# Kernel tuning notes

Measured on AMD Instinct MI355X. Metric: run time of the kernel, lower is better.

Reference implementation:

```python
import jax, jax.numpy as jnp
import numpy as np

S = 16384   # num src nodes
D = 16384   # num dst nodes
FS = 128    # src feature len
FD = 128    # dst feature len
R = 50.0    # dist threshold (m)
L = 2005.0  # box side so avg degree ~ 32
LN_EPS = 1e-5


def setup_inputs() -> dict:
    rng = np.random.default_rng(0)
    src_pos_np = rng.uniform(0.0, L, (S, 2)).astype(np.float32)
    dst_pos_np = rng.uniform(0.0, L, (D, 2)).astype(np.float32)
    # radius-graph edge construction (data-dependent, done once outside jit)
    es, ed = [], []
    CH = 2048
    for i in range(0, S, CH):
        d = np.linalg.norm(src_pos_np[i:i + CH, None, :] - dst_pos_np[None, :, :], axis=-1)
        si, di = np.nonzero(d <= R)
        es.append((si + i).astype(np.int32))
        ed.append(di.astype(np.int32))
    edge_src_idx = jnp.asarray(np.concatenate(es))
    edge_dst_idx = jnp.asarray(np.concatenate(ed))

    key = jax.random.key(0)
    ks = jax.random.split(key, 12)
    w = lambda k, shape: (jax.random.normal(k, shape, jnp.float32) * 0.02)
    return {
        'src_node_features': jax.random.normal(ks[0], (S, FS), jnp.float32),
        'src_node_pos': jnp.asarray(src_pos_np),
        'dst_node_features': jax.random.normal(ks[1], (D, FD), jnp.float32),
        'dst_node_pos': jnp.asarray(dst_pos_np),
        'src_w': w(ks[2], (FS, FS)), 'src_b': jnp.zeros((FS,), jnp.float32),
        'dst_w': w(ks[3], (FD, FD)), 'dst_b': jnp.zeros((FD,), jnp.float32),
        'dist_w': w(ks[4], (2, FD)), 'dist_b': jnp.zeros((FD,), jnp.float32),
        'edge_w1': w(ks[5], (FS + FD + FD, FD)), 'edge_b1': jnp.zeros((FD,), jnp.float32),
        'edge_w2': w(ks[6], (FD, FD)), 'edge_b2': jnp.zeros((FD,), jnp.float32),
        'ln_g': jnp.ones((FD,), jnp.float32), 'ln_b': jnp.zeros((FD,), jnp.float32),
        'out_w': w(ks[7], (FD, FD)), 'out_b': jnp.zeros((FD,), jnp.float32),
        'edge_src_idx': edge_src_idx,
        'edge_dst_idx': edge_dst_idx,
    }


def reference(src_node_features, src_node_pos, dst_node_features, dst_node_pos,
              src_w, src_b, dst_w, dst_b, dist_w, dist_b,
              edge_w1, edge_b1, edge_w2, edge_b2, ln_g, ln_b, out_w, out_b,
              edge_src_idx, edge_dst_idx):
    # node encoders: Linear + ReLU
    src_enc = jax.nn.relu(src_node_features @ src_w + src_b)   # [S, FS]
    dst_enc = jax.nn.relu(dst_node_features @ dst_w + dst_b)   # [D, FD]
    # gather per-edge
    e_src = src_enc[edge_src_idx]                               # [E, FS]
    e_dst = dst_enc[edge_dst_idx]                               # [E, FD]
    e_dpos = src_node_pos[edge_src_idx] - dst_node_pos[edge_dst_idx]  # [E, 2]
    e_dist = jax.nn.relu(e_dpos @ dist_w + dist_b)              # [E, FD]
    # edge MLP: Linear-ReLU-Linear on concat [E, FS+FD+FD]
    e_in = jnp.concatenate([e_src, e_dist, e_dst], axis=-1)
    e_out = jax.nn.relu(e_in @ edge_w1 + edge_b1) @ edge_w2 + edge_b2  # [E, FD]
    # scatter-add to destination nodes
    agg = dst_enc + jax.ops.segment_sum(e_out, edge_dst_idx, num_segments=D)
    # LayerNorm + ReLU + Linear + residual + ReLU
    mu = jnp.mean(agg, axis=-1, keepdims=True)
    var = jnp.mean(jnp.square(agg - mu), axis=-1, keepdims=True)
    ln = (agg - mu) * jax.lax.rsqrt(var + LN_EPS) * ln_g + ln_b
    h = jax.nn.relu(ln) @ out_w + out_b + dst_node_features
    return jax.nn.relu(h)
```

## Files before the change

### kernel.cpp

```cpp
#include <hip/hip_runtime.h>

typedef unsigned short ushort_t;
typedef unsigned int uint_t;
typedef short bhalf8 __attribute__((ext_vector_type(8)));
typedef float f32x4 __attribute__((ext_vector_type(4)));

__device__ __forceinline__ float b2f(ushort_t u) {
    union { uint_t i; float f; } v; v.i = ((uint_t)u) << 16; return v.f;
}
__device__ __forceinline__ ushort_t f2b(float f) {
    union { float f; uint_t i; } v; v.f = f;
    uint_t r = v.i + 0x7fffu + ((v.i >> 16) & 1u);
    return (ushort_t)(r >> 16);
}
__device__ __forceinline__ uint_t addpack_trunc(uint_t a, uint_t b) {
    union { uint_t i; float f; } t0, t1, s0, s1;
    t0.i = a << 16;          s0.i = b << 16;
    t1.i = a & 0xffff0000u;  s1.i = b & 0xffff0000u;
    float lo = t0.f + s0.f, hi = t1.f + s1.f;
    union { float f; uint_t i; } rl, rh; rl.f = lo; rh.f = hi;
    return (rl.i >> 16) | (rh.i & 0xffff0000u);
}

__global__ __launch_bounds__(256) void prep_kernel(
    const float* __restrict__ wsrc, const float* __restrict__ wdst,
    const float* __restrict__ w2,   const float* __restrict__ wout,
    const float* __restrict__ w1,
    ushort_t* __restrict__ msrc, ushort_t* __restrict__ mdst,
    ushort_t* __restrict__ m2,   ushort_t* __restrict__ mout,
    ushort_t* __restrict__ m1a,  ushort_t* __restrict__ m1b,
    ushort_t* __restrict__ m1c,
    const int* __restrict__ edi, int E, int* __restrict__ deg,
    float* __restrict__ hsum, int countB, int zeroB, int Dn)
{
    int b = blockIdx.x, tid = threadIdx.x;
    if (b < 56) {
        const float* ins[7] = { wsrc, wdst, w2, wout, w1, w1 + 128*128, w1 + 256*128 };
        ushort_t* outs[7]   = { msrc, mdst, m2, mout, m1a, m1b, m1c };
        int mat = b >> 3;
        const float* in = ins[mat];
        ushort_t* out = outs[mat];
        int flat = (b & 7)*256 + tid;
        int nt = flat >> 8, rem = flat & 255;
        int ks = rem >> 6, lane = rem & 63;
        int q = lane >> 4, m = lane & 15;
        #pragma unroll
        for (int j = 0; j < 8; ++j)
            out[flat*8 + j] = f2b(in[(ks*32 + q*8 + j)*128 + nt*16 + m]);
    } else if (b < 56 + countB) {
        int i = (b - 56)*256 + tid;
        if (i < E) atomicAdd(&deg[edi[i]], 1);
    } else {
        int zb = b - 56 - countB;
        float4* h4 = (float4*)hsum;
        int total4 = Dn*32;
        for (int i = zb*256 + tid; i < total4; i += zeroB*256)
            h4[i] = make_float4(0.f, 0.f, 0.f, 0.f);
    }
}

__global__ __launch_bounds__(256) void enc2_kernel(
    const float* __restrict__ src_feat, const float* __restrict__ dst_feat,
    const ushort_t* __restrict__ msrc, const ushort_t* __restrict__ mdst,
    const ushort_t* __restrict__ m1a,  const ushort_t* __restrict__ m1c,
    const float* __restrict__ src_b,   const float* __restrict__ dst_b,
    ushort_t* __restrict__ Csrc, ushort_t* __restrict__ Cdst,
    ushort_t* __restrict__ dst_enc, int Sb)
{
    __shared__ ushort_t A_l[64*136];
    __shared__ ushort_t E_l[64*136];
    __shared__ float b_l[128];
    int tid = threadIdx.x, blk = blockIdx.x;

    const float* A; const ushort_t *W1m, *W2m; const float* bias;
    ushort_t *outC, *outEnc; int rowbase;
    if (blk < Sb) { A = src_feat; W1m = msrc; W2m = m1a; bias = src_b;
                    outC = Csrc; outEnc = nullptr; rowbase = blk*64; }
    else          { A = dst_feat; W1m = mdst; W2m = m1c; bias = dst_b;
                    outC = Cdst; outEnc = dst_enc; rowbase = (blk - Sb)*64; }

    const float4* A4 = (const float4*)A;
    for (int i = tid; i < 2048; i += 256) {
        int r = i >> 5, c = i & 31;
        float4 v = A4[(size_t)(rowbase + r)*32 + c];
        uint2 u;
        u.x = (uint_t)f2b(v.x) | ((uint_t)f2b(v.y) << 16);
        u.y = (uint_t)f2b(v.z) | ((uint_t)f2b(v.w) << 16);
        *(uint2*)(A_l + r*136 + c*4) = u;
    }
    if (tid < 128) b_l[tid] = bias[tid];
    __syncthreads();

    int lane = tid & 63, w = tid >> 6, q = lane >> 4, m = lane & 15;
    const bhalf8* Wv1 = (const bhalf8*)W1m;
    f32x4 acc[4][2] = {};
    #pragma unroll
    for (int ks = 0; ks < 4; ++ks) {
        bhalf8 bf0 = Wv1[((2*w)*4 + ks)*64 + lane];
        bhalf8 bf1 = Wv1[((2*w+1)*4 + ks)*64 + lane];
        #pragma unroll
        for (int mt = 0; mt < 4; ++mt) {
            bhalf8 a = *(const bhalf8*)(A_l + (mt*16 + m)*136 + ks*32 + q*8);
            acc[mt][0] = __builtin_amdgcn_mfma_f32_16x16x32_bf16(a, bf0, acc[mt][0], 0, 0, 0);
            acc[mt][1] = __builtin_amdgcn_mfma_f32_16x16x32_bf16(a, bf1, acc[mt][1], 0, 0, 0);
        }
    }
    #pragma unroll
    for (int mt = 0; mt < 4; ++mt)
    #pragma unroll
    for (int nt = 0; nt < 2; ++nt)
    #pragma unroll
    for (int reg = 0; reg < 4; ++reg) {
        int col = w*32 + nt*16 + m;
        int row = mt*16 + q*4 + reg;
        ushort_t e = f2b(fmaxf(acc[mt][nt][reg] + b_l[col], 0.f));
        E_l[row*136 + col] = e;
        if (outEnc) outEnc[(size_t)(rowbase + row)*128 + col] = e;
    }
    __syncthreads();

    const bhalf8* Wv2 = (const bhalf8*)W2m;
    f32x4 acc2[4][2] = {};
    #pragma unroll
    for (int ks = 0; ks < 4; ++ks) {
        bhalf8 bf0 = Wv2[((2*w)*4 + ks)*64 + lane];
        bhalf8 bf1 = Wv2[((2*w+1)*4 + ks)*64 + lane];
        #pragma unroll
        for (int mt = 0; mt < 4; ++mt) {
            bhalf8 a = *(const bhalf8*)(E_l + (mt*16 + m)*136 + ks*32 + q*8);
            acc2[mt][0] = __builtin_amdgcn_mfma_f32_16x16x32_bf16(a, bf0, acc2[mt][0], 0, 0, 0);
            acc2[mt][1] = __builtin_amdgcn_mfma_f32_16x16x32_bf16(a, bf1, acc2[mt][1], 0, 0, 0);
        }
    }
    #pragma unroll
    for (int mt = 0; mt < 4; ++mt)
    #pragma unroll
    for (int nt = 0; nt < 2; ++nt)
    #pragma unroll
    for (int reg = 0; reg < 4; ++reg) {
        int col = w*32 + nt*16 + m;
        int row = mt*16 + q*4 + reg;
        outC[(size_t)(rowbase + row)*128 + col] = f2b(acc2[mt][nt][reg]);
    }
}

__global__ __launch_bounds__(1024) void scan_deg(const int* __restrict__ deg,
                                                 int* __restrict__ nxt, int Dn)
{
    __shared__ int sums[1024];
    int t = threadIdx.x;
    int per = Dn >> 10;
    const int4* d4 = (const int4*)(deg + t*per);
    int4 v[4]; int s = 0;
    #pragma unroll
    for (int k = 0; k < 4; ++k) { v[k] = d4[k]; s += v[k].x + v[k].y + v[k].z + v[k].w; }
    sums[t] = s;
    __syncthreads();
    for (int off = 1; off < 1024; off <<= 1) {
        int x = (t >= off) ? sums[t - off] : 0;
        __syncthreads();
        sums[t] += x;
        __syncthreads();
    }
    int run = sums[t] - s;
    int4* n4 = (int4*)(nxt + t*per);
    #pragma unroll
    for (int k = 0; k < 4; ++k) {
        int4 o;
        o.x = run; run += v[k].x;
        o.y = run; run += v[k].y;
        o.z = run; run += v[k].z;
        o.w = run; run += v[k].w;
        n4[k] = o;
    }
}

__global__ __launch_bounds__(256) void fill_sorted(
    const int* __restrict__ esi, const int* __restrict__ edi, int E,
    int* __restrict__ nxt, int* __restrict__ ss, int* __restrict__ sd)
{
    int i = blockIdx.x*256 + threadIdx.x;
    if (i < E) {
        int s = esi[i], d = edi[i];
        int p = atomicAdd(&nxt[d], 1);
        ss[p] = s; sd[p] = d;
    }
}

__global__ __launch_bounds__(256, 4) void edge_kernel(
    const ushort_t* __restrict__ Csrc, const ushort_t* __restrict__ Cdst,
    const float* __restrict__ src_pos, const float* __restrict__ dst_pos,
    const int* __restrict__ sorted_s, const int* __restrict__ sorted_d, int E,
    const ushort_t* __restrict__ w1bm, const float* __restrict__ eb1,
    const float* __restrict__ dist_w, const float* __restrict__ dist_b,
    float* __restrict__ hsum)
{
    __shared__ ushort_t X[64*136];
    __shared__ ushort_t G_l[64*136];
    __shared__ int s_l[64], ed_l[64], dv_l[64];
    __shared__ float dx_l[64], dy_l[64];
    __shared__ float b1_l[128], dw0_l[128], dw1_l[128], db_l[128];

    int tid = threadIdx.x, blk = blockIdx.x;

    if (tid < 64) {
        int slot = blk*64 + tid;
        if (slot < E) {
            int s = sorted_s[slot], d = sorted_d[slot];
            s_l[tid] = s; ed_l[tid] = d; dv_l[tid] = d;
            float2 sp = ((const float2*)src_pos)[s];
            float2 dp = ((const float2*)dst_pos)[d];
            dx_l[tid] = sp.x - dp.x;
            dy_l[tid] = sp.y - dp.y;
        } else {
            s_l[tid] = 0; ed_l[tid] = 0x7fffffff; dv_l[tid] = 0;
            dx_l[tid] = 0.f; dy_l[tid] = 0.f;
        }
    }
    if (tid < 128) {
        b1_l[tid]  = eb1[tid];
        dw0_l[tid] = dist_w[tid];
        dw1_l[tid] = dist_w[128 + tid];
        db_l[tid]  = dist_b[tid];
    }
    __syncthreads();

    const uint4* cs4 = (const uint4*)Csrc;
    const uint4* cd4 = (const uint4*)Cdst;
    for (int i = tid; i < 1024; i += 256) {
        int r = i >> 4, c = i & 15;
        uint4 a = cs4[(size_t)s_l[r]*16 + c];
        uint4 b = cd4[(size_t)dv_l[r]*16 + c];
        uint4 u;
        u.x = addpack_trunc(a.x, b.x);
        u.y = addpack_trunc(a.y, b.y);
        u.z = addpack_trunc(a.z, b.z);
        u.w = addpack_trunc(a.w, b.w);
        *(uint4*)(G_l + r*136 + c*8) = u;
    }
    for (int i = tid; i < 4096; i += 256) {
        int r = i >> 6, j2 = (i & 63)*2;
        float dx = dx_l[r], dy = dy_l[r];
        float v0 = fmaxf(dx*dw0_l[j2]   + dy*dw1_l[j2]   + db_l[j2],   0.f);
        float v1 = fmaxf(dx*dw0_l[j2+1] + dy*dw1_l[j2+1] + db_l[j2+1], 0.f);
        *(uint_t*)(X + r*136 + j2) = (uint_t)f2b(v0) | ((uint_t)f2b(v1) << 16);
    }
    __syncthreads();

    int lane = tid & 63, w = tid >> 6, q = lane >> 4, m = lane & 15;
    f32x4 acc[4][2] = {};
    const bhalf8* Wv = (const bhalf8*)w1bm;
    #pragma unroll
    for (int ks = 0; ks < 4; ++ks) {
        bhalf8 bf0 = Wv[((2*w)*4 + ks)*64 + lane];
        bhalf8 bf1 = Wv[((2*w+1)*4 + ks)*64 + lane];
        #pragma unroll
        for (int mt = 0; mt < 4; ++mt) {
            bhalf8 a = *(const bhalf8*)(X + (mt*16 + m)*136 + ks*32 + q*8);
            acc[mt][0] = __builtin_amdgcn_mfma_f32_16x16x32_bf16(a, bf0, acc[mt][0], 0, 0, 0);
            acc[mt][1] = __builtin_amdgcn_mfma_f32_16x16x32_bf16(a, bf1, acc[mt][1], 0, 0, 0);
        }
    }
    __syncthreads();

    #pragma unroll
    for (int mt = 0; mt < 4; ++mt)
    #pragma unroll
    for (int reg = 0; reg < 4; ++reg) {
        int row = mt*16 + q*4 + reg;
        #pragma unroll
        for (int nt = 0; nt < 2; ++nt) {
            int col = w*32 + nt*16 + m;
            float v = acc[mt][nt][reg] + b1_l[col] + b2f(G_l[row*136 + col]);
            X[row*136 + col] = f2b(fmaxf(v, 0.f));
        }
    }
    __syncthreads();

    {
        int j = tid & 127, h = tid >> 7;
        int rend = h*32 + 32;
        float a = 0.f;
        for (int r = h*32; r < rend; ++r) {
            a += b2f(X[r*136 + j]);
            int dcur = ed_l[r];
            bool bnd = (r == rend - 1) || (ed_l[r + 1] != dcur);
            if (bnd) {
                if (dcur != 0x7fffffff) atomicAdd(&hsum[(size_t)dcur*128 + j], a);
                a = 0.f;
            }
        }
    }
}

__global__ __launch_bounds__(256) void aggfinal_kernel(
    const float* __restrict__ hsum, const ushort_t* __restrict__ w2m,
    const float* __restrict__ b2, const int* __restrict__ deg,
    const ushort_t* __restrict__ dst_enc, const float* __restrict__ ln_g,
    const float* __restrict__ ln_b, const ushort_t* __restrict__ moutm,
    const float* __restrict__ out_b, const float* __restrict__ dst_feat,
    float* __restrict__ out)
{
    __shared__ char buf[64*132*4];
    __shared__ ushort_t act_l[64*136];
    __shared__ float b2_l[128], g_l[128], bl_l[128], ob_l[128];
    __shared__ int deg_l[64];
    __shared__ float ps[64][4], ps2[64][4], mu_l[64], inv_l[64];

    ushort_t* A_l = (ushort_t*)buf;
    float* Y = (float*)buf;
    int tid = threadIdx.x, blk = blockIdx.x;

    const float4* hv = (const float4*)hsum;
    for (int i = tid; i < 1024; i += 256) {
        int r = i >> 4, c = i & 15;
        size_t base = (size_t)(blk*64 + r)*32 + c*2;
        float4 p0 = hv[base], p1 = hv[base + 1];
        uint4 u;
        u.x = (uint_t)f2b(p0.x) | ((uint_t)f2b(p0.y) << 16);
        u.y = (uint_t)f2b(p0.z) | ((uint_t)f2b(p0.w) << 16);
        u.z = (uint_t)f2b(p1.x) | ((uint_t)f2b(p1.y) << 16);
        u.w = (uint_t)f2b(p1.z) | ((uint_t)f2b(p1.w) << 16);
        *(uint4*)(A_l + r*136 + c*8) = u;
    }
    if (tid < 128) { b2_l[tid] = b2[tid]; g_l[tid] = ln_g[tid];
                     bl_l[tid] = ln_b[tid]; ob_l[tid] = out_b[tid]; }
    if (tid < 64) deg_l[tid] = deg[blk*64 + tid];
    __syncthreads();

    int lane = tid & 63, w = tid >> 6, q = lane >> 4, m = lane & 15;
    f32x4 acc[4][2] = {};
    const bhalf8* Wv = (const bhalf8*)w2m;
    #pragma unroll
    for (int ks = 0; ks < 4; ++ks) {
        bhalf8 bf0 = Wv[((2*w)*4 + ks)*64 + lane];
        bhalf8 bf1 = Wv[((2*w+1)*4 + ks)*64 + lane];
        #pragma unroll
        for (int mt = 0; mt < 4; ++mt) {
            bhalf8 a = *(const bhalf8*)(A_l + (mt*16 + m)*136 + ks*32 + q*8);
            acc[mt][0] = __builtin_amdgcn_mfma_f32_16x16x32_bf16(a, bf0, acc[mt][0], 0, 0, 0);
            acc[mt][1] = __builtin_amdgcn_mfma_f32_16x16x32_bf16(a, bf1, acc[mt][1], 0, 0, 0);
        }
    }
    __syncthreads();

    #pragma unroll
    for (int mt = 0; mt < 4; ++mt)
    #pragma unroll
    for (int nt = 0; nt < 2; ++nt)
    #pragma unroll
    for (int reg = 0; reg < 4; ++reg) {
        int col = w*32 + nt*16 + m;
        int rowl = mt*16 + q*4 + reg;
        size_t grow = (size_t)blk*64 + rowl;
        float v = acc[mt][nt][reg] + (float)deg_l[rowl]*b2_l[col] + b2f(dst_enc[grow*128 + col]);
        Y[rowl*132 + col] = v;
    }
    __syncthreads();

    {
        int r = tid >> 2, t4 = tid & 3;
        float s = 0.f, s2 = 0.f;
        for (int jj = 0; jj < 32; ++jj) {
            float v = Y[r*132 + t4*32 + jj];
            s += v; s2 += v*v;
        }
        ps[r][t4] = s; ps2[r][t4] = s2;
    }
    __syncthreads();
    if (tid < 64) {
        int r = tid;
        float sum = ps[r][0] + ps[r][1] + ps[r][2] + ps[r][3];
        float sum2 = ps2[r][0] + ps2[r][1] + ps2[r][2] + ps2[r][3];
        float mu = sum / 128.f;
        float var = sum2 / 128.f - mu*mu;
        mu_l[r] = mu;
        inv_l[r] = 1.0f / sqrtf(var + 1e-5f);
    }
    __syncthreads();
    for (int i = tid; i < 4096; i += 256) {
        int r = i >> 6, j2 = (i & 63)*2;
        float v0 = fmaxf((Y[r*132 + j2]   - mu_l[r]) * inv_l[r] * g_l[j2]   + bl_l[j2],   0.f);
        float v1 = fmaxf((Y[r*132 + j2+1] - mu_l[r]) * inv_l[r] * g_l[j2+1] + bl_l[j2+1], 0.f);
        *(uint_t*)(act_l + r*136 + j2) = (uint_t)f2b(v0) | ((uint_t)f2b(v1) << 16);
    }
    __syncthreads();

    f32x4 acc2[4][2] = {};
    const bhalf8* Wo = (const bhalf8*)moutm;
    #pragma unroll
    for (int ks = 0; ks < 4; ++ks) {
        bhalf8 bf0 = Wo[((2*w)*4 + ks)*64 + lane];
        bhalf8 bf1 = Wo[((2*w+1)*4 + ks)*64 + lane];
        #pragma unroll
        for (int mt = 0; mt < 4; ++mt) {
            bhalf8 a = *(const bhalf8*)(act_l + (mt*16 + m)*136 + ks*32 + q*8);
            acc2[mt][0] = __builtin_amdgcn_mfma_f32_16x16x32_bf16(a, bf0, acc2[mt][0], 0, 0, 0);
            acc2[mt][1] = __builtin_amdgcn_mfma_f32_16x16x32_bf16(a, bf1, acc2[mt][1], 0, 0, 0);
        }
    }
    #pragma unroll
    for (int mt = 0; mt < 4; ++mt)
    #pragma unroll
    for (int nt = 0; nt < 2; ++nt)
    #pragma unroll
    for (int reg = 0; reg < 4; ++reg) {
        int col = w*32 + nt*16 + m;
        size_t row = (size_t)blk*64 + mt*16 + q*4 + reg;
        float v = acc2[mt][nt][reg] + ob_l[col] + dst_feat[row*128 + col];
        out[row*128 + col] = fmaxf(v, 0.f);
    }
}

extern "C" void kernel_launch(void* const* d_in, const int* in_sizes, int n_in,
                              void* d_out, int out_size, void* d_ws, size_t ws_size,
                              hipStream_t stream)
{
    const float* src_feat = (const float*)d_in[0];
    const float* src_pos  = (const float*)d_in[1];
    const float* dst_feat = (const float*)d_in[2];
    const float* dst_pos  = (const float*)d_in[3];
    const float* src_w    = (const float*)d_in[4];
    const float* src_b    = (const float*)d_in[5];
    const float* dst_w    = (const float*)d_in[6];
    const float* dst_b    = (const float*)d_in[7];
    const float* dist_w   = (const float*)d_in[8];
    const float* dist_b   = (const float*)d_in[9];
    const float* w1       = (const float*)d_in[10];
    const float* b1       = (const float*)d_in[11];
    const float* w2       = (const float*)d_in[12];
    const float* b2       = (const float*)d_in[13];
    const float* ln_g     = (const float*)d_in[14];
    const float* ln_b     = (const float*)d_in[15];
    const float* out_w    = (const float*)d_in[16];
    const float* out_b    = (const float*)d_in[17];
    const int* esi        = (const int*)d_in[18];
    const int* edi        = (const int*)d_in[19];
    int E = in_sizes[18];
    int S = in_sizes[0] / 128;
    int D = in_sizes[2] / 128;

    char* ws = (char*)d_ws;
    size_t off = 0;
    auto alloc = [&](size_t bytes) { char* p = ws + off; off += (bytes + 511) & ~(size_t)511; return p; };
    ushort_t* Csrc    = (ushort_t*)alloc((size_t)S*128*2);
    ushort_t* Cdst    = (ushort_t*)alloc((size_t)D*128*2);
    ushort_t* dst_enc = (ushort_t*)alloc((size_t)D*128*2);
    float*    hsum    = (float*)   alloc((size_t)D*128*4);
    ushort_t* msrc    = (ushort_t*)alloc(128*128*2);
    ushort_t* mdst    = (ushort_t*)alloc(128*128*2);
    ushort_t* m2      = (ushort_t*)alloc(128*128*2);
    ushort_t* mout    = (ushort_t*)alloc(128*128*2);
    ushort_t* m1a     = (ushort_t*)alloc(128*128*2);
    ushort_t* m1b     = (ushort_t*)alloc(128*128*2);
    ushort_t* m1c     = (ushort_t*)alloc(128*128*2);
    int*      deg     = (int*)     alloc((size_t)D*4);
    int*      nxt     = (int*)     alloc((size_t)D*4);
    int*      ss      = (int*)     alloc((size_t)E*4);
    int*      sd      = (int*)     alloc((size_t)E*4);

    hipMemsetAsync(deg, 0, (size_t)D*4, stream);

    int countB = (E + 255)/256;
    int zeroB = 256;
    prep_kernel<<<56 + countB + zeroB, 256, 0, stream>>>(
        src_w, dst_w, w2, out_w, w1,
        msrc, mdst, m2, mout, m1a, m1b, m1c,
        edi, E, deg, hsum, countB, zeroB, D);

    int Sb = S/64, Db = D/64;
    enc2_kernel<<<Sb + Db, 256, 0, stream>>>(
        src_feat, dst_feat, msrc, mdst, m1a, m1c, src_b, dst_b,
        Csrc, Cdst, dst_enc, Sb);

    scan_deg<<<1, 1024, 0, stream>>>(deg, nxt, D);
    fill_sorted<<<(E + 255)/256, 256, 0, stream>>>(esi, edi, E, nxt, ss, sd);

    edge_kernel<<<(E + 63)/64, 256, 0, stream>>>(
        Csrc, Cdst, src_pos, dst_pos, ss, sd, E,
        m1b, b1, dist_w, dist_b, hsum);

    aggfinal_kernel<<<Db, 256, 0, stream>>>(
        hsum, m2, b2, deg, dst_enc, ln_g, ln_b,
        mout, out_b, dst_feat, (float*)d_out);
}
```

Baseline: 247.5 us.

## Fuse degree scan into encoder, pack sorted edges, keep edge hidden in fp32 LDS

Folds the single-block degree prefix scan into the encoder launch as an extra block, removing one kernel launch. Moves the edge bias b1 into the precomputed dst-side projection, and stores the sorted (src,dst) pairs as one int2 array. In the edge kernel, the ReLU hidden values are kept in fp32 shared memory aliased over the X/G buffers instead of being rounded back to bf16, and segment boundaries and destination offsets are precomputed once per block. The scan block now uses 256 threads with 16 int4 loads each, and the distance features use truncating bf16 packing, which slightly changes rounding.

```diff
diff --git a/kernel.cpp b/kernel.cpp
--- a/kernel.cpp
+++ b/kernel.cpp
@@ -13,13 +13,17 @@
     uint_t r = v.i + 0x7fffu + ((v.i >> 16) & 1u);
     return (ushort_t)(r >> 16);
 }
+__device__ __forceinline__ uint_t f2u(float f) {
+    union { float f; uint_t i; } v; v.f = f; return v.i;
+}
+__device__ __forceinline__ uint_t pack_trunc(float lo, float hi) {
+    return (f2u(lo) >> 16) | (f2u(hi) & 0xffff0000u);
+}
 __device__ __forceinline__ uint_t addpack_trunc(uint_t a, uint_t b) {
     union { uint_t i; float f; } t0, t1, s0, s1;
     t0.i = a << 16;          s0.i = b << 16;
     t1.i = a & 0xffff0000u;  s1.i = b & 0xffff0000u;
-    float lo = t0.f + s0.f, hi = t1.f + s1.f;
-    union { float f; uint_t i; } rl, rh; rl.f = lo; rh.f = hi;
-    return (rl.i >> 16) | (rh.i & 0xffff0000u);
+    return pack_trunc(t0.f + s0.f, t1.f + s1.f);
 }
 
 __global__ __launch_bounds__(256) void prep_kernel(
@@ -64,20 +68,54 @@
     const ushort_t* __restrict__ msrc, const ushort_t* __restrict__ mdst,
     const ushort_t* __restrict__ m1a,  const ushort_t* __restrict__ m1c,
     const float* __restrict__ src_b,   const float* __restrict__ dst_b,
+    const float* __restrict__ b1,
     ushort_t* __restrict__ Csrc, ushort_t* __restrict__ Cdst,
-    ushort_t* __restrict__ dst_enc, int Sb)
+    ushort_t* __restrict__ dst_enc,
+    const int* __restrict__ deg, int* __restrict__ nxt, int Dn,
+    int Sb, int Db)
 {
+    int tid = threadIdx.x, blk = blockIdx.x;
+
+    if (blk == Sb + Db) {
+        __shared__ int sums[256];
+        int per = Dn >> 8;
+        const int4* d4 = (const int4*)(deg + tid*per);
+        int4 v[16]; int s = 0;
+        #pragma unroll
+        for (int k = 0; k < 16; ++k) { v[k] = d4[k]; s += v[k].x + v[k].y + v[k].z + v[k].w; }
+        sums[tid] = s;
+        __syncthreads();
+        for (int off = 1; off < 256; off <<= 1) {
+            int x = (tid >= off) ? sums[tid - off] : 0;
+            __syncthreads();
+            sums[tid] += x;
+            __syncthreads();
+        }
+        int run = sums[tid] - s;
+        int4* n4 = (int4*)(nxt + tid*per);
+        #pragma unroll
+        for (int k = 0; k < 16; ++k) {
+            int4 o;
+            o.x = run; run += v[k].x;
+            o.y = run; run += v[k].y;
+            o.z = run; run += v[k].z;
+            o.w = run; run += v[k].w;
+            n4[k] = o;
+        }
+        return;
+    }
+
     __shared__ ushort_t A_l[64*136];
     __shared__ ushort_t E_l[64*136];
     __shared__ float b_l[128];
-    int tid = threadIdx.x, blk = blockIdx.x;
+    __shared__ float b2_l[128];
 
     const float* A; const ushort_t *W1m, *W2m; const float* bias;
-    ushort_t *outC, *outEnc; int rowbase;
+    ushort_t *outC, *outEnc; int rowbase; const float* bias2;
     if (blk < Sb) { A = src_feat; W1m = msrc; W2m = m1a; bias = src_b;
-                    outC = Csrc; outEnc = nullptr; rowbase = blk*64; }
+                    outC = Csrc; outEnc = nullptr; rowbase = blk*64; bias2 = nullptr; }
     else          { A = dst_feat; W1m = mdst; W2m = m1c; bias = dst_b;
-                    outC = Cdst; outEnc = dst_enc; rowbase = (blk - Sb)*64; }
+                    outC = Cdst; outEnc = dst_enc; rowbase = (blk - Sb)*64; bias2 = b1; }
 
     const float4* A4 = (const float4*)A;
     for (int i = tid; i < 2048; i += 256) {
@@ -88,7 +126,7 @@
         u.y = (uint_t)f2b(v.z) | ((uint_t)f2b(v.w) << 16);
         *(uint2*)(A_l + r*136 + c*4) = u;
     }
-    if (tid < 128) b_l[tid] = bias[tid];
+    if (tid < 128) { b_l[tid] = bias[tid]; b2_l[tid] = bias2 ? bias2[tid] : 0.f; }
     __syncthreads();
 
     int lane = tid & 63, w = tid >> 6, q = lane >> 4, m = lane & 15;
@@ -140,91 +178,68 @@
     for (int reg = 0; reg < 4; ++reg) {
         int col = w*32 + nt*16 + m;
         int row = mt*16 + q*4 + reg;
-        outC[(size_t)(rowbase + row)*128 + col] = f2b(acc2[mt][nt][reg]);
-    }
-}
-
-__global__ __launch_bounds__(1024) void scan_deg(const int* __restrict__ deg,
-                                                 int* __restrict__ nxt, int Dn)
-{
-    __shared__ int sums[1024];
-    int t = threadIdx.x;
-    int per = Dn >> 10;
-    const int4* d4 = (const int4*)(deg + t*per);
-    int4 v[4]; int s = 0;
-    #pragma unroll
-    for (int k = 0; k < 4; ++k) { v[k] = d4[k]; s += v[k].x + v[k].y + v[k].z + v[k].w; }
-    sums[t] = s;
-    __syncthreads();
-    for (int off = 1; off < 1024; off <<= 1) {
-        int x = (t >= off) ? sums[t - off] : 0;
-        __syncthreads();
-        sums[t] += x;
-        __syncthreads();
-    }
-    int run = sums[t] - s;
-    int4* n4 = (int4*)(nxt + t*per);
-    #pragma unroll
-    for (int k = 0; k < 4; ++k) {
-        int4 o;
-        o.x = run; run += v[k].x;
-        o.y = run; run += v[k].y;
-        o.z = run; run += v[k].z;
-        o.w = run; run += v[k].w;
-        n4[k] = o;
+        outC[(size_t)(rowbase + row)*128 + col] = f2b(acc2[mt][nt][reg] + b2_l[col]);
     }
 }
 
 __global__ __launch_bounds__(256) void fill_sorted(
     const int* __restrict__ esi, const int* __restrict__ edi, int E,
-    int* __restrict__ nxt, int* __restrict__ ss, int* __restrict__ sd)
+    int* __restrict__ nxt, int2* __restrict__ spair)
 {
     int i = blockIdx.x*256 + threadIdx.x;
     if (i < E) {
         int s = esi[i], d = edi[i];
         int p = atomicAdd(&nxt[d], 1);
-        ss[p] = s; sd[p] = d;
+        spair[p] = make_int2(s, d);
     }
 }
 
 __global__ __launch_bounds__(256, 4) void edge_kernel(
     const ushort_t* __restrict__ Csrc, const ushort_t* __restrict__ Cdst,
     const float* __restrict__ src_pos, const float* __restrict__ dst_pos,
-    const int* __restrict__ sorted_s, const int* __restrict__ sorted_d, int E,
-    const ushort_t* __restrict__ w1bm, const float* __restrict__ eb1,
+    const int2* __restrict__ spair, int E,
+    const ushort_t* __restrict__ w1bm,
     const float* __restrict__ dist_w, const float* __restrict__ dist_b,
     float* __restrict__ hsum)
 {
-    __shared__ ushort_t X[64*136];
-    __shared__ ushort_t G_l[64*136];
-    __shared__ int s_l[64], ed_l[64], dv_l[64];
+    __shared__ char pool[34816];
+    __shared__ int s_l[64], d_l[64], dv_l[64], bnd_l[64], dofs_l[64];
     __shared__ float dx_l[64], dy_l[64];
-    __shared__ float b1_l[128], dw0_l[128], dw1_l[128], db_l[128];
+    __shared__ float dw0_l[128], dw1_l[128], db_l[128];
+
+    ushort_t* X = (ushort_t*)pool;
+    ushort_t* G = (ushort_t*)(pool + 17408);
+    float* H = (float*)pool;
 
     int tid = threadIdx.x, blk = blockIdx.x;
 
     if (tid < 64) {
         int slot = blk*64 + tid;
         if (slot < E) {
-            int s = sorted_s[slot], d = sorted_d[slot];
-            s_l[tid] = s; ed_l[tid] = d; dv_l[tid] = d;
-            float2 sp = ((const float2*)src_pos)[s];
-            float2 dp = ((const float2*)dst_pos)[d];
+            int2 pr = spair[slot];
+            s_l[tid] = pr.x; d_l[tid] = pr.y; dv_l[tid] = pr.y;
+            float2 sp = ((const float2*)src_pos)[pr.x];
+            float2 dp = ((const float2*)dst_pos)[pr.y];
             dx_l[tid] = sp.x - dp.x;
             dy_l[tid] = sp.y - dp.y;
         } else {
-            s_l[tid] = 0; ed_l[tid] = 0x7fffffff; dv_l[tid] = 0;
+            s_l[tid] = 0; d_l[tid] = -1; dv_l[tid] = 0;
             dx_l[tid] = 0.f; dy_l[tid] = 0.f;
         }
     }
     if (tid < 128) {
-        b1_l[tid]  = eb1[tid];
         dw0_l[tid] = dist_w[tid];
         dw1_l[tid] = dist_w[128 + tid];
         db_l[tid]  = dist_b[tid];
     }
     __syncthreads();
 
+    if (tid < 64) {
+        int d = d_l[tid];
+        int dn = (tid < 63) ? d_l[tid + 1] : -2;
+        bnd_l[tid] = (tid == 31) || (tid == 63) || (dn != d);
+        dofs_l[tid] = (d >= 0) ? d*128 : -1;
+    }
     const uint4* cs4 = (const uint4*)Csrc;
     const uint4* cd4 = (const uint4*)Cdst;
     for (int i = tid; i < 1024; i += 256) {
@@ -236,14 +251,14 @@
         u.y = addpack_trunc(a.y, b.y);
         u.z = addpack_trunc(a.z, b.z);
         u.w = addpack_trunc(a.w, b.w);
-        *(uint4*)(G_l + r*136 + c*8) = u;
+        *(uint4*)(G + r*136 + c*8) = u;
     }
     for (int i = tid; i < 4096; i += 256) {
         int r = i >> 6, j2 = (i & 63)*2;
         float dx = dx_l[r], dy = dy_l[r];
-        float v0 = fmaxf(dx*dw0_l[j2]   + dy*dw1_l[j2]   + db_l[j2],   0.f);
-        float v1 = fmaxf(dx*dw0_l[j2+1] + dy*dw1_l[j2+1] + db_l[j2+1], 0.f);
-        *(uint_t*)(X + r*136 + j2) = (uint_t)f2b(v0) | ((uint_t)f2b(v1) << 16);
+        float v0 = fmaxf(fmaf(dx, dw0_l[j2],   fmaf(dy, dw1_l[j2],   db_l[j2])),   0.f);
+        float v1 = fmaxf(fmaf(dx, dw0_l[j2+1], fmaf(dy, dw1_l[j2+1], db_l[j2+1])), 0.f);
+        *(uint_t*)(X + r*136 + j2) = pack_trunc(v0, v1);
     }
     __syncthreads();
 
@@ -264,15 +279,37 @@
     __syncthreads();
 
     #pragma unroll
-    for (int mt = 0; mt < 4; ++mt)
+    for (int mt = 0; mt < 2; ++mt)
     #pragma unroll
     for (int reg = 0; reg < 4; ++reg) {
         int row = mt*16 + q*4 + reg;
         #pragma unroll
         for (int nt = 0; nt < 2; ++nt) {
             int col = w*32 + nt*16 + m;
-            float v = acc[mt][nt][reg] + b1_l[col] + b2f(G_l[row*136 + col]);
-            X[row*136 + col] = f2b(fmaxf(v, 0.f));
+            H[row*132 + col] = fmaxf(acc[mt][nt][reg] + b2f(G[row*136 + col]), 0.f);
+        }
+    }
+    float gv[2][4][2];
+    #pragma unroll
+    for (int mt = 2; mt < 4; ++mt)
+    #pragma unroll
+    for (int reg = 0; reg < 4; ++reg) {
+        int row = mt*16 + q*4 + reg;
+        #pragma unroll
+        for (int nt = 0; nt < 2; ++nt)
+            gv[mt-2][reg][nt] = b2f(G[row*136 + w*32 + nt*16 + m]);
+    }
+    __syncthreads();
+
+    #pragma unroll
+    for (int mt = 2; mt < 4; ++mt)
+    #pragma unroll
+    for (int reg = 0; reg < 4; ++reg) {
+        int row = mt*16 + q*4 + reg;
+        #pragma unroll
+        for (int nt = 0; nt < 2; ++nt) {
+            int col = w*32 + nt*16 + m;
+            H[row*132 + col] = fmaxf(acc[mt][nt][reg] + gv[mt-2][reg][nt], 0.f);
         }
     }
     __syncthreads();
@@ -282,11 +319,10 @@
         int rend = h*32 + 32;
         float a = 0.f;
         for (int r = h*32; r < rend; ++r) {
-            a += b2f(X[r*136 + j]);
-            int dcur = ed_l[r];
-            bool bnd = (r == rend - 1) || (ed_l[r + 1] != dcur);
-            if (bnd) {
-                if (dcur != 0x7fffffff) atomicAdd(&hsum[(size_t)dcur*128 + j], a);
+            a += H[r*132 + j];
+            if (bnd_l[r]) {
+                int ofs = dofs_l[r];
+                if (ofs >= 0) atomicAdd(&hsum[(size_t)ofs + j], a);
                 a = 0.f;
             }
         }
@@ -456,8 +492,7 @@
     ushort_t* m1c     = (ushort_t*)alloc(128*128*2);
     int*      deg     = (int*)     alloc((size_t)D*4);
     int*      nxt     = (int*)     alloc((size_t)D*4);
-    int*      ss      = (int*)     alloc((size_t)E*4);
-    int*      sd      = (int*)     alloc((size_t)E*4);
+    int2*     spair   = (int2*)    alloc((size_t)E*8);
 
     hipMemsetAsync(deg, 0, (size_t)D*4, stream);
 
@@ -469,16 +504,15 @@
         edi, E, deg, hsum, countB, zeroB, D);
 
     int Sb = S/64, Db = D/64;
-    enc2_kernel<<<Sb + Db, 256, 0, stream>>>(
-        src_feat, dst_feat, msrc, mdst, m1a, m1c, src_b, dst_b,
-        Csrc, Cdst, dst_enc, Sb);
-
-    scan_deg<<<1, 1024, 0, stream>>>(deg, nxt, D);
-    fill_sorted<<<(E + 255)/256, 256, 0, stream>>>(esi, edi, E, nxt, ss, sd);
+    enc2_kernel<<<Sb + Db + 1, 256, 0, stream>>>(
+        src_feat, dst_feat, msrc, mdst, m1a, m1c, src_b, dst_b, b1,
+        Csrc, Cdst, dst_enc, deg, nxt, D, Sb, Db);
+
+    fill_sorted<<<(E + 255)/256, 256, 0, stream>>>(esi, edi, E, nxt, spair);
 
     edge_kernel<<<(E + 63)/64, 256, 0, stream>>>(
-        Csrc, Cdst, src_pos, dst_pos, ss, sd, E,
-        m1b, b1, dist_w, dist_b, hsum);
+        Csrc, Cdst, src_pos, dst_pos, spair, E,
+        m1b, dist_w, dist_b, hsum);
 
     aggfinal_kernel<<<Db, 256, 0, stream>>>(
         hsum, m2, b2, deg, dst_enc, ln_g, ln_b,
```

Result: faster. 234.2 us (-5.4%).
